# Performance work log

Hardware: AMD Instinct MI355X
Metric: run time of the kernel (lower is better)

## Reference

```python
import jax, jax.numpy as jnp
import numpy as np
import math
from itertools import combinations

SEQ_LEN = 8
SET_SIZE = 3
IN_DIM = 2048
OUT_DIM = 1152
WAY = 5
SHOT = 5
N_QUERIES = 200
PE_SCALE = 0.1
LN_EPS = 1e-5
NEG_INF = -1e30

TUPLES = np.array(list(combinations(range(SEQ_LEN), SET_SIZE)), dtype=np.int32)  # [56, 3]
TUPLES_LEN = TUPLES.shape[0]


def _positional_encoding(d_model, max_len):
    position = np.arange(max_len)[:, None].astype(np.float32)
    div_term = np.exp(np.arange(0, d_model, 2).astype(np.float32) * -(math.log(10000.0) / d_model))
    pe = np.zeros((max_len, d_model), dtype=np.float32)
    pe[:, 0::2] = np.sin(position * div_term) * PE_SCALE
    pe[:, 1::2] = np.cos(position * div_term) * PE_SCALE
    return jnp.asarray(pe)

PE = _positional_encoding(IN_DIM, int(SEQ_LEN * 1.5))


def setup_inputs() -> dict:
    key = jax.random.key(0)
    ks = jax.random.split(key, 6)
    support_set = jax.random.normal(ks[0], (WAY * SHOT, SEQ_LEN, IN_DIM), dtype=jnp.float32)
    queries = jax.random.normal(ks[1], (N_QUERIES, SEQ_LEN, IN_DIM), dtype=jnp.float32)
    support_labels = jnp.repeat(jnp.arange(WAY, dtype=jnp.int32), SHOT)  # [25]
    Wk = jax.random.normal(ks[2], (IN_DIM * SET_SIZE, OUT_DIM), dtype=jnp.float32) * 0.02
    bk = jnp.zeros((OUT_DIM,), dtype=jnp.float32)
    Wv = jax.random.normal(ks[3], (IN_DIM * SET_SIZE, OUT_DIM), dtype=jnp.float32) * 0.02
    bv = jnp.zeros((OUT_DIM,), dtype=jnp.float32)
    ln_g = jnp.ones((OUT_DIM,), dtype=jnp.float32)
    ln_b = jnp.zeros((OUT_DIM,), dtype=jnp.float32)
    return {"support_set": support_set, "support_labels": support_labels, "queries": queries,
            "Wk": Wk, "bk": bk, "Wv": Wv, "bv": bv, "ln_g": ln_g, "ln_b": ln_b}


def _layernorm(x, g, b):
    mu = jnp.mean(x, axis=-1, keepdims=True)
    var = jnp.var(x, axis=-1, keepdims=True)
    return (x - mu) * jax.lax.rsqrt(var + LN_EPS) * g + b


def _tuple_features(x):
    # x: [N, SEQ_LEN, IN_DIM]; add PE (dropout is identity at inference), gather frame tuples.
    n = x.shape[0]
    x = x + PE[None, :x.shape[1], :]
    return x[:, TUPLES, :].reshape(n, TUPLES_LEN, SET_SIZE * IN_DIM)  # [N, 56, 6144]


def reference(support_set, support_labels, queries, Wk, bk, Wv, bv, ln_g, ln_b):
    n_q = queries.shape[0]
    s_feat = _tuple_features(support_set)   # [S, T, 6144]
    q_feat = _tuple_features(queries)       # [Q, T, 6144]

    sk = _layernorm(s_feat @ Wk + bk, ln_g, ln_b)  # [S, T, D]
    qk = _layernorm(q_feat @ Wk + bk, ln_g, ln_b)  # [Q, T, D]
    sv = s_feat @ Wv + bv                           # [S, T, D]
    qv = q_feat @ Wv + bv                           # [Q, T, D]

    # scores between every query tuple and every support tuple
    scores = jnp.einsum('qtd,skd->qtsk', qk, sk) / math.sqrt(OUT_DIM)  # [Q, T, S, T]

    # per-class masked softmax over (support clips of class c) x (support tuples)
    class_mask = support_labels[None, :] == jnp.arange(WAY, dtype=support_labels.dtype)[:, None]  # [WAY, S]
    masked = scores[None] + jnp.where(class_mask[:, None, None, :, None], 0.0, NEG_INF)  # [WAY, Q, T, S, T]
    attn = jax.nn.softmax(masked.reshape(WAY, n_q, TUPLES_LEN, -1), axis=-1)
    attn = attn.reshape(WAY, n_q, TUPLES_LEN, -1, TUPLES_LEN)  # [WAY, Q, T, S, T]

    proto = jnp.einsum('cqtsk,skd->cqtd', attn, sv)  # [WAY, Q, T, D]
    diff = qv[None] - proto                           # [WAY, Q, T, D]
    dist = -jnp.sum(diff * diff, axis=(2, 3)) / TUPLES_LEN  # [WAY, Q]
    return dist.T  # logits [Q, WAY]
```

## Files before the change

kernel.cpp:

```cpp
#include <hip/hip_runtime.h>
#include <math.h>

#define SEQ_LEN 8
#define IN_DIM 2048
#define OUT_DIM 1152
#define NTUP 56
#define NSUP 25
#define NQ 200
#define WAY 5
#define SFRAMES 200
#define NFRAMES 1800
#define SROWS 1400
#define QROWS 11200
#define AT_STRIDE 1440
#define KC 288
#define ALD 296

typedef __attribute__((ext_vector_type(8))) short short8;
typedef __attribute__((ext_vector_type(4))) float f32x4;

__device__ __constant__ int TUP[NTUP][3] = {
{0,1,2},{0,1,3},{0,1,4},{0,1,5},{0,1,6},{0,1,7},
{0,2,3},{0,2,4},{0,2,5},{0,2,6},{0,2,7},
{0,3,4},{0,3,5},{0,3,6},{0,3,7},
{0,4,5},{0,4,6},{0,4,7},
{0,5,6},{0,5,7},
{0,6,7},
{1,2,3},{1,2,4},{1,2,5},{1,2,6},{1,2,7},
{1,3,4},{1,3,5},{1,3,6},{1,3,7},
{1,4,5},{1,4,6},{1,4,7},
{1,5,6},{1,5,7},
{1,6,7},
{2,3,4},{2,3,5},{2,3,6},{2,3,7},
{2,4,5},{2,4,6},{2,4,7},
{2,5,6},{2,5,7},
{2,6,7},
{3,4,5},{3,4,6},{3,4,7},
{3,5,6},{3,5,7},
{3,6,7},
{4,5,6},{4,5,7},
{4,6,7},
{5,6,7}};

__device__ __forceinline__ unsigned short f2bf(float x) {
  union { float f; unsigned int u; } v; v.f = x;
  unsigned int r = v.u + 0x7fffu + ((v.u >> 16) & 1u);
  return (unsigned short)(r >> 16);
}
__device__ __forceinline__ float bf2f(unsigned short s) {
  union { float f; unsigned int u; } v; v.u = ((unsigned int)s) << 16;
  return v.f;
}

__device__ __forceinline__ void gll16(const void* g, void* l) {
  __builtin_amdgcn_global_load_lds(
      (const __attribute__((address_space(1))) unsigned int*)g,
      (__attribute__((address_space(3))) unsigned int*)l, 16, 0, 0);
}

#define VMCNT(N) asm volatile("s_waitcnt vmcnt(" #N ")" ::: "memory")

__device__ __forceinline__ void pbar() {
  asm volatile("" ::: "memory");
  __builtin_amdgcn_s_barrier();
  asm volatile("" ::: "memory");
}

#define APB_OFF   0UL
#define WT_OFF    7372800UL
#define PB_OFF    35684352UL
#define QKB_OFF   60567552UL
#define SKB_OFF   86372352UL
#define QVB_OFF   89597952UL
#define SVB_OFF   115402752UL
#define G2_OFF    118628352UL
#define SCB_OFF   119457792UL
#define G1B_OFF   151713792UL
#define QNORM_OFF 183969792UL
#define RANK_OFF  184014592UL

__global__ __launch_bounds__(256) void k_pre(const float* __restrict__ S,
                                             const float* __restrict__ Q,
                                             const float* __restrict__ Wk,
                                             const float* __restrict__ Wv,
                                             const int* __restrict__ labels,
                                             unsigned short* __restrict__ APb,
                                             unsigned short* __restrict__ WT,
                                             int* __restrict__ rank,
                                             float* __restrict__ outz) {
  __shared__ float t[32][33];
  int b = blockIdx.x, tid = threadIdx.x;
  if (b < NFRAMES) {
    int frame = b;
    int e8 = tid * 8;
    int pos = frame & 7;
    const float c0 = -logf(10000.0f) / (float)IN_DIM;
    float pe[8];
#pragma unroll
    for (int p = 0; p < 4; ++p) {
      float dt = expf((float)(e8 + 2 * p) * c0);
      float arg = (float)pos * dt;
      pe[2 * p] = sinf(arg) * 0.1f;
      pe[2 * p + 1] = cosf(arg) * 0.1f;
    }
    const float* src = (frame < SFRAMES) ? (S + (size_t)frame * IN_DIM + e8)
                                         : (Q + (size_t)(frame - SFRAMES) * IN_DIM + e8);
    float4 x0 = ((const float4*)src)[0], x1 = ((const float4*)src)[1];
    short8 o;
    o[0] = (short)f2bf(x0.x + pe[0]); o[1] = (short)f2bf(x0.y + pe[1]);
    o[2] = (short)f2bf(x0.z + pe[2]); o[3] = (short)f2bf(x0.w + pe[3]);
    o[4] = (short)f2bf(x1.x + pe[4]); o[5] = (short)f2bf(x1.y + pe[5]);
    o[6] = (short)f2bf(x1.z + pe[6]); o[7] = (short)f2bf(x1.w + pe[7]);
    *(short8*)(APb + (size_t)frame * IN_DIM + e8) = o;
  } else if (b < NFRAMES + 13824) {
    int z = b - NFRAMES;
    int bz = z / (64 * 36); int rem = z % (64 * 36);
    int by = rem / 64, bx = rem % 64;
    int w = bz / 3, j = bz % 3;
    const float* W = w ? Wv : Wk;
    int k0 = bx * 32, d0 = by * 32;
    int tx = tid & 31, ty = tid >> 5;
#pragma unroll
    for (int i = 0; i < 4; ++i) {
      int k = k0 + ty + i * 8;
      t[ty + i * 8][tx] = W[(size_t)(j * IN_DIM + k) * OUT_DIM + d0 + tx];
    }
    __syncthreads();
    int colbase = w * 3456 + j * 1152 + d0;
#pragma unroll
    for (int i = 0; i < 4; ++i) {
      int d = ty + i * 8;
      WT[(size_t)(colbase + d) * IN_DIM + k0 + tx] = f2bf(t[tx][d]);
    }
  } else {
    for (int i = tid; i < NQ * WAY; i += 256) outz[i] = 0.f;
    if (tid == 0) {
      for (int s = 0; s < NSUP; ++s) {
        int r = 0;
        for (int s2 = 0; s2 < NSUP; ++s2)
          r += (labels[s2] < labels[s]) || (labels[s2] == labels[s] && s2 < s);
        rank[s] = r;
      }
    }
  }
}

__device__ __forceinline__ void mfma_core256(const short* __restrict__ A, int lda, int maxA,
                                             const short* __restrict__ B, int ldb, int maxB,
                                             int K, short* lds, f32x4 (&acc)[8][4]) {
  int tid = threadIdx.x;
  int lane = tid & 63, wave = tid >> 6;
  int wm = wave >> 1, wn = wave & 1;
  int col = lane & 15, quad = lane >> 4;
  int kq8 = (quad ^ ((col >> 1) & 3)) * 8;

  int rt_ = tid >> 2;
  int qo = ((tid & 3) ^ ((tid >> 3) & 3)) * 8;
  const short* a0p = A + (size_t)min(rt_,       maxA) * lda + qo;
  const short* a1p = A + (size_t)min(rt_ + 64,  maxA) * lda + qo;
  const short* a2p = A + (size_t)min(rt_ + 128, maxA) * lda + qo;
  const short* a3p = A + (size_t)min(rt_ + 192, maxA) * lda + qo;
  const short* b0p = B + (size_t)min(rt_,       maxB) * ldb + qo;
  const short* b1p = B + (size_t)min(rt_ + 64,  maxB) * ldb + qo;
  const int nt = K >> 5;

#define STAGE(t, cb)                                 \
  do {                                               \
    short* buf_ = lds + (cb);                        \
    int k0_ = (t) << 5;                              \
    gll16(a0p + k0_, buf_ + (size_t)tid * 8);        \
    gll16(a1p + k0_, buf_ + (size_t)(tid + 256) * 8);\
    gll16(a2p + k0_, buf_ + (size_t)(tid + 512) * 8);\
    gll16(a3p + k0_, buf_ + (size_t)(tid + 768) * 8);\
    gll16(b0p + k0_, buf_ + 8192 + (size_t)tid * 8); \
    gll16(b1p + k0_, buf_ + 8192 + (size_t)(tid + 256) * 8);\
  } while (0)

  STAGE(0, 0);
  STAGE(1, 12288);
  VMCNT(6);
  pbar();
  int c0 = 0, c1 = 12288, c2 = 24576;
  for (int t = 0; t < nt; ++t) {
    if (t + 2 < nt) STAGE(t + 2, c2);
    const short* As = lds + c0;
    const short* Bs = As + 8192;
    short8 af[8], bf[4];
#pragma unroll
    for (int i = 0; i < 8; ++i)
      af[i] = *(const short8*)(As + (wm * 128 + i * 16 + col) * 32 + kq8);
#pragma unroll
    for (int j = 0; j < 4; ++j)
      bf[j] = *(const short8*)(Bs + (wn * 64 + j * 16 + col) * 32 + kq8);
    __builtin_amdgcn_s_setprio(1);
#pragma unroll
    for (int i = 0; i < 8; ++i)
#pragma unroll
      for (int j = 0; j < 4; ++j)
        acc[i][j] = __builtin_amdgcn_mfma_f32_16x16x32_bf16(af[i], bf[j], acc[i][j], 0, 0, 0);
    __builtin_amdgcn_s_setprio(0);
    if (t + 2 < nt)      VMCNT(6);
    else if (t + 1 < nt) VMCNT(0);
    pbar();
    int tmp = c0; c0 = c1; c1 = c2; c2 = tmp;
  }
#undef STAGE
}

__global__ __launch_bounds__(256, 2) void k_gemm1(const unsigned short* __restrict__ APb,
                                                  const unsigned short* __restrict__ WT,
                                                  unsigned short* __restrict__ Pb) {
  __shared__ short lds[36864];
  int o = blockIdx.x;
  int L = (o & 7) * 54 + (o >> 3);
  int rt = L / 54, ct = L % 54;
  int row0 = rt << 8, col0 = ct << 7;
  f32x4 acc[8][4];
#pragma unroll
  for (int i = 0; i < 8; ++i)
#pragma unroll
    for (int j = 0; j < 4; ++j) acc[i][j] = (f32x4)(0.f);
  mfma_core256((const short*)APb + (size_t)row0 * IN_DIM, IN_DIM, min(255, NFRAMES - 1 - row0),
               (const short*)WT + (size_t)col0 * IN_DIM, IN_DIM, 127,
               IN_DIM, lds, acc);
  int lane = threadIdx.x & 63, wave = threadIdx.x >> 6;
  int wm = wave >> 1, wn = wave & 1, col = lane & 15, quad = lane >> 4;
#pragma unroll
  for (int i = 0; i < 8; ++i)
#pragma unroll
    for (int r = 0; r < 4; ++r) {
      int gr = row0 + wm * 128 + i * 16 + quad * 4 + r;
      if (gr >= NFRAMES) continue;
#pragma unroll
      for (int j = 0; j < 4; ++j)
        Pb[(size_t)gr * 6912 + col0 + wn * 64 + j * 16 + col] = f2bf(acc[i][j][r]);
    }
}

__global__ __launch_bounds__(256) void k_combine(const unsigned short* __restrict__ Pb,
                                                 const float* __restrict__ bk,
                                                 const float* __restrict__ bv,
                                                 const float* __restrict__ g,
                                                 const float* __restrict__ bb,
                                                 const int* __restrict__ rank,
                                                 unsigned short* __restrict__ SKb,
                                                 unsigned short* __restrict__ QKb,
                                                 unsigned short* __restrict__ SVb,
                                                 unsigned short* __restrict__ QVb,
                                                 float* __restrict__ qnorm) {
  __shared__ short L[8 * 3456];
  int n = blockIdx.x, w = blockIdx.y;
  int tid = threadIdx.x;
  bool sup = n < NSUP;
  int fbase = sup ? n * SEQ_LEN : SFRAMES + (n - NSUP) * SEQ_LEN;
  for (int i = 0; i < 14; ++i) {
    int idx = tid + 256 * i;
    if (idx < 3456) {
      int fr = idx / 432, off = (idx - fr * 432) * 8;
      *(short8*)(L + fr * 3456 + off) =
          *(const short8*)(Pb + (size_t)(fbase + fr) * 6912 + w * 3456 + off);
    }
  }
  __syncthreads();
  int wave = tid >> 6, lane = tid & 63;
  const float* bias = w ? bv : bk;
  float2 bi[9], gg[9], bbv[9];
#pragma unroll
  for (int i = 0; i < 9; ++i) {
    int p = lane + 64 * i;
    bi[i] = *(const float2*)(bias + 2 * p);
    if (w == 0) {
      gg[i] = *(const float2*)(g + 2 * p);
      bbv[i] = *(const float2*)(bb + 2 * p);
    }
  }
  int obase = sup ? rank[n] * NTUP : (n - NSUP) * NTUP;
  const unsigned int* Lu = (const unsigned int*)L;
  for (int t = wave; t < NTUP; t += 4) {
    int b0 = (TUP[t][0] * 3456) >> 1;
    int b1 = (TUP[t][1] * 3456 + 1152) >> 1;
    int b2 = (TUP[t][2] * 3456 + 2304) >> 1;
    float va[18];
    float sum = 0.f, sq = 0.f;
#pragma unroll
    for (int i = 0; i < 9; ++i) {
      int p = lane + 64 * i;
      unsigned int u0 = Lu[b0 + p], u1 = Lu[b1 + p], u2 = Lu[b2 + p];
      float a = bf2f((unsigned short)u0) + bf2f((unsigned short)u1) +
                bf2f((unsigned short)u2) + bi[i].x;
      float b = bf2f((unsigned short)(u0 >> 16)) + bf2f((unsigned short)(u1 >> 16)) +
                bf2f((unsigned short)(u2 >> 16)) + bi[i].y;
      va[2 * i] = a; va[2 * i + 1] = b;
      sum += a + b;
      sq += a * a + b * b;
    }
#pragma unroll
    for (int o = 32; o; o >>= 1) {
      sum += __shfl_xor(sum, o);
      sq += __shfl_xor(sq, o);
    }
    int orow = obase + t;
    if (w == 0) {
      float mean = sum * (1.f / OUT_DIM);
      float var = sq * (1.f / OUT_DIM) - mean * mean;
      float inv = rsqrtf(var + 1e-5f);
      unsigned short* outp = (sup ? SKb : QKb) + (size_t)orow * OUT_DIM;
#pragma unroll
      for (int i = 0; i < 9; ++i) {
        int p = lane + 64 * i;
        unsigned int lo = f2bf((va[2 * i] - mean) * inv * gg[i].x + bbv[i].x);
        unsigned int hi = f2bf((va[2 * i + 1] - mean) * inv * gg[i].y + bbv[i].y);
        *(unsigned int*)(outp + 2 * p) = lo | (hi << 16);
      }
    } else {
      unsigned short* outp = (sup ? SVb : QVb) + (size_t)orow * OUT_DIM;
#pragma unroll
      for (int i = 0; i < 9; ++i) {
        int p = lane + 64 * i;
        unsigned int lo = f2bf(va[2 * i]);
        unsigned int hi = f2bf(va[2 * i + 1]);
        *(unsigned int*)(outp + 2 * p) = lo | (hi << 16);
      }
      if (!sup && lane == 0) qnorm[orow] = sq;
    }
  }
}

__global__ __launch_bounds__(256, 2) void k_rowgemm(const unsigned short* __restrict__ QKb,
                                                    const unsigned short* __restrict__ SKb,
                                                    const unsigned short* __restrict__ QVb,
                                                    const unsigned short* __restrict__ SVb,
                                                    unsigned short* __restrict__ SCb,
                                                    unsigned short* __restrict__ G1b,
                                                    unsigned short* __restrict__ G2) {
  __shared__ short lds[36864];
  int o = blockIdx.x;
  int xcd = o & 7, idx = o >> 3;
  int L = (xcd < 6 ? xcd * 125 : 750 + (xcd - 6) * 124) + idx;
  f32x4 acc[8][4];
#pragma unroll
  for (int i = 0; i < 8; ++i)
#pragma unroll
    for (int j = 0; j < 4; ++j) acc[i][j] = (f32x4)(0.f);
  int lane = threadIdx.x & 63, wave = threadIdx.x >> 6;
  int wm = wave >> 1, wn = wave & 1, col = lane & 15, quad = lane >> 4;

  if (L < 968) {
    int g1 = L >= 484; int l = g1 ? L - 484 : L;
    int rt = l / 11, ct = l % 11;
    int row0 = rt << 8, col0 = ct << 7;
    const unsigned short* Am = g1 ? QVb : QKb;
    const unsigned short* Bm = g1 ? SVb : SKb;
    mfma_core256((const short*)Am + (size_t)row0 * OUT_DIM, OUT_DIM, min(255, QROWS - 1 - row0),
                 (const short*)Bm + (size_t)col0 * OUT_DIM, OUT_DIM, min(127, SROWS - 1 - col0),
                 OUT_DIM, lds, acc);
    unsigned short* outp = g1 ? G1b : SCb;
    const float scl = g1 ? 1.0f : 0.029462782549439483f;
#pragma unroll
    for (int i = 0; i < 8; ++i)
#pragma unroll
      for (int r = 0; r < 4; ++r) {
        int gr = row0 + wm * 128 + i * 16 + quad * 4 + r;
        if (gr >= QROWS) continue;
#pragma unroll
        for (int j = 0; j < 4; ++j) {
          int gc = col0 + wn * 64 + j * 16 + col;
          if (gc < SROWS) {
            int c = gc / 280;
            outp[(size_t)gr * AT_STRIDE + gc + c * 8] = f2bf(acc[i][j][r] * scl);
          }
        }
      }
  } else {
    int l = L - 968;
    int c = l / 6, rem = l % 6;
    int rt = rem / 3, ct = rem % 3;
    int i0 = rt << 8, j0 = ct << 7;
    const short* base = (const short*)SVb + (size_t)c * 280 * OUT_DIM;
    mfma_core256(base + (size_t)i0 * OUT_DIM, OUT_DIM, 279 - i0,
                 base + (size_t)j0 * OUT_DIM, OUT_DIM, min(127, 279 - j0),
                 OUT_DIM, lds, acc);
    unsigned short* g2c = G2 + (size_t)c * KC * KC;
#pragma unroll
    for (int i = 0; i < 8; ++i)
#pragma unroll
      for (int r = 0; r < 4; ++r) {
        int gi = i0 + wm * 128 + i * 16 + quad * 4 + r;
        if (gi >= KC) continue;
#pragma unroll
        for (int j = 0; j < 4; ++j) {
          int gj = j0 + wn * 64 + j * 16 + col;
          if (gj < KC) g2c[(size_t)gi * KC + gj] = f2bf(acc[i][j][r]);
        }
      }
  }
}

__global__ __launch_bounds__(256) void k_attn(const unsigned short* __restrict__ SCb,
                                              const unsigned short* __restrict__ G1b,
                                              const unsigned short* __restrict__ G2,
                                              const float* __restrict__ qnorm,
                                              float* __restrict__ out) {
  __shared__ short attn[64 * ALD];
  __shared__ float T2n[64];
  __shared__ float Sarr[64];
  __shared__ float rowsum[64];
  __shared__ float val[64];
  int r0 = blockIdx.x * 64, c = blockIdx.y;
  int tid = threadIdx.x;

  int lr = tid >> 2, h = tid & 3;
  const unsigned short* ps = SCb + (size_t)(r0 + lr) * AT_STRIDE + c * KC;
  const unsigned short* pg = G1b + (size_t)(r0 + lr) * AT_STRIDE + c * KC;
  short8 sv[9];
  float mx = -INFINITY;
#pragma unroll
  for (int i = 0; i < 9; ++i) {
    int v = h * 9 + i;
    if (v < 35) {
      sv[i] = *(const short8*)(ps + v * 8);
#pragma unroll
      for (int j = 0; j < 8; ++j) mx = fmaxf(mx, bf2f((unsigned short)sv[i][j]));
    }
  }
  mx = fmaxf(mx, __shfl_xor(mx, 1));
  mx = fmaxf(mx, __shfl_xor(mx, 2));
  float sum = 0.f, t2 = 0.f;
#pragma unroll
  for (int i = 0; i < 9; ++i) {
    int v = h * 9 + i;
    if (v < 35) {
      short8 gv8 = *(const short8*)(pg + v * 8);
      short8 e8;
#pragma unroll
      for (int j = 0; j < 8; ++j) {
        float e = __expf(bf2f((unsigned short)sv[i][j]) - mx);
        sum += e;
        t2 += e * bf2f((unsigned short)gv8[j]);
        e8[j] = (short)f2bf(e);
      }
      *(short8*)(attn + lr * ALD + v * 8) = e8;
    } else {
      *(short8*)(attn + lr * ALD + v * 8) = (short8)0;
    }
  }
  sum += __shfl_xor(sum, 1); sum += __shfl_xor(sum, 2);
  t2 += __shfl_xor(t2, 1); t2 += __shfl_xor(t2, 2);
  if (h == 0) { Sarr[lr] = sum; T2n[lr] = t2; }
  if (tid < 64) rowsum[tid] = 0.f;
  __syncthreads();

  int lane = tid & 63, wave = tid >> 6;
  int col = lane & 15, quad = lane >> 4;
  const short* G2c = (const short*)G2 + (size_t)c * KC * KC;
  float part[4][4] = {};
  for (int j0 = 0; j0 < KC; j0 += 64) {
    int ncols = min(64, KC - j0);
    if (wave * 16 < ncols) {
      const short* brow = G2c + (size_t)(j0 + wave * 16 + col) * KC + quad * 8;
      f32x4 acc[4];
#pragma unroll
      for (int i = 0; i < 4; ++i) acc[i] = (f32x4)(0.f);
      for (int kq = 0; kq < 9; ++kq) {
        short8 bf = *(const short8*)(brow + kq * 32);
#pragma unroll
        for (int i = 0; i < 4; ++i) {
          short8 af = *(const short8*)(attn + (i * 16 + col) * ALD + kq * 32 + quad * 8);
          acc[i] = __builtin_amdgcn_mfma_f32_16x16x32_bf16(af, bf, acc[i], 0, 0, 0);
        }
      }
      int gcol = j0 + wave * 16 + col;
#pragma unroll
      for (int i = 0; i < 4; ++i)
#pragma unroll
        for (int r = 0; r < 4; ++r)
          part[i][r] += bf2f((unsigned short)attn[(i * 16 + quad * 4 + r) * ALD + gcol]) *
                        acc[i][r];
    }
  }
#pragma unroll
  for (int i = 0; i < 4; ++i)
#pragma unroll
    for (int r = 0; r < 4; ++r) {
      float s = part[i][r];
      s += __shfl_xor(s, 1); s += __shfl_xor(s, 2);
      s += __shfl_xor(s, 4); s += __shfl_xor(s, 8);
      if (col == 0) atomicAdd(&rowsum[i * 16 + quad * 4 + r], s);
    }
  __syncthreads();

  if (tid < 64) {
    float S = Sarr[tid], invS = 1.f / S;
    val[tid] = qnorm[r0 + tid] - 2.f * T2n[tid] * invS + rowsum[tid] * invS * invS;
  }
  __syncthreads();
  if (tid < 3) {
    int q = r0 / NTUP + tid;
    int lo = max(q * NTUP, r0), hi = min(q * NTUP + NTUP, r0 + 64);
    if (lo < hi && q < NQ) {
      float s = 0.f;
      for (int r = lo; r < hi; ++r) s += val[r - r0];
      atomicAdd(&out[q * WAY + c], -s * (1.f / NTUP));
    }
  }
}

extern "C" void kernel_launch(void* const* d_in, const int* in_sizes, int n_in,
                              void* d_out, int out_size, void* d_ws, size_t ws_size,
                              hipStream_t stream) {
  const float* support = (const float*)d_in[0];
  const int* labels = (const int*)d_in[1];
  const float* queries = (const float*)d_in[2];
  const float* Wk = (const float*)d_in[3];
  const float* bk = (const float*)d_in[4];
  const float* Wv = (const float*)d_in[5];
  const float* bv = (const float*)d_in[6];
  const float* ln_g = (const float*)d_in[7];
  const float* ln_b = (const float*)d_in[8];
  float* out = (float*)d_out;
  char* w8 = (char*)d_ws;

  unsigned short* APb = (unsigned short*)(w8 + APB_OFF);
  unsigned short* WT = (unsigned short*)(w8 + WT_OFF);
  unsigned short* Pb = (unsigned short*)(w8 + PB_OFF);
  unsigned short* QKb = (unsigned short*)(w8 + QKB_OFF);
  unsigned short* SKb = (unsigned short*)(w8 + SKB_OFF);
  unsigned short* QVb = (unsigned short*)(w8 + QVB_OFF);
  unsigned short* SVb = (unsigned short*)(w8 + SVB_OFF);
  unsigned short* G2 = (unsigned short*)(w8 + G2_OFF);
  unsigned short* SCb = (unsigned short*)(w8 + SCB_OFF);
  unsigned short* G1b = (unsigned short*)(w8 + G1B_OFF);
  float* QNORM = (float*)(w8 + QNORM_OFF);
  int* RANK = (int*)(w8 + RANK_OFF);

  k_pre<<<dim3(NFRAMES + 13824 + 1), dim3(256), 0, stream>>>(support, queries, Wk, Wv,
                                                             labels, APb, WT, RANK, out);
  k_gemm1<<<dim3(432), dim3(256), 0, stream>>>(APb, WT, Pb);
  k_combine<<<dim3(225, 2), dim3(256), 0, stream>>>(Pb, bk, bv, ln_g, ln_b, RANK,
                                                    SKb, QKb, SVb, QVb, QNORM);
  k_rowgemm<<<dim3(998), dim3(256), 0, stream>>>(QKb, SKb, QVb, SVb, SCb, G1b, G2);
  k_attn<<<dim3(175, 5), dim3(256), 0, stream>>>(SCb, G1b, G2, QNORM, out);
}
```

Measured before the change: 342.0 us.

## Compute query-support value Gram from per-frame projection products instead of tuple rows

Instead of forming the full 11200x1400 QV·SV^T GEMM over tuple rows, the query and support value projections are packed per frame (three 1152-wide chunks per frame) and a much smaller 4800x600 frame-level GEMM is computed. A new assembly kernel then reconstructs each tuple-pair dot product by summing the frame-chunk products plus the bias cross-terms. This exploits the tuple structure to drop about 484 GEMM tiles, and the tuple-level QV matrix is no longer written. In exchange it adds two extra kernel launches, an fp32 intermediate buffer, and a scattered assembly pass.

```diff
diff --git a/kernel.cpp b/kernel.cpp
--- a/kernel.cpp
+++ b/kernel.cpp
@@ -71,7 +71,10 @@
 #define PB_OFF    35684352UL
 #define QKB_OFF   60567552UL
 #define SKB_OFF   86372352UL
-#define QVB_OFF   89597952UL
+#define AQ_OFF    89597952UL
+#define AS_OFF    100657152UL
+#define PVB_OFF   102039552UL
+#define H_OFF     102061312UL
 #define SVB_OFF   115402752UL
 #define G2_OFF    118628352UL
 #define SCB_OFF   119457792UL
@@ -237,6 +240,34 @@
     }
 }
 
+__global__ __launch_bounds__(256) void k_pack(const unsigned short* __restrict__ Pb,
+                                              const float* __restrict__ bv,
+                                              const int* __restrict__ rank,
+                                              unsigned short* __restrict__ Aq,
+                                              unsigned short* __restrict__ As,
+                                              float* __restrict__ pvb) {
+  int fr = blockIdx.x, tid = threadIdx.x;
+  const unsigned short* src = Pb + (size_t)fr * 6912 + 3456;
+  unsigned short* dst;
+  if (fr < SFRAMES) {
+    int n = fr >> 3, f = fr & 7;
+    dst = As + ((size_t)rank[n] * 8 + f) * 3456;
+  } else {
+    dst = Aq + (size_t)(fr - SFRAMES) * 3456;
+  }
+  for (int i = tid; i < 432; i += 256)
+    *(short8*)(dst + i * 8) = *(const short8*)(src + i * 8);
+  int wave = tid >> 6, lane = tid & 63;
+  if (wave < 3) {
+    float s = 0.f;
+    for (int k = lane; k < OUT_DIM; k += 64)
+      s += bf2f(src[wave * 1152 + k]) * bv[k];
+#pragma unroll
+    for (int o = 32; o; o >>= 1) s += __shfl_xor(s, o);
+    if (lane == 0) pvb[fr * 3 + wave] = s;
+  }
+}
+
 __global__ __launch_bounds__(256) void k_combine(const unsigned short* __restrict__ Pb,
                                                  const float* __restrict__ bk,
                                                  const float* __restrict__ bv,
@@ -246,7 +277,6 @@
                                                  unsigned short* __restrict__ SKb,
                                                  unsigned short* __restrict__ QKb,
                                                  unsigned short* __restrict__ SVb,
-                                                 unsigned short* __restrict__ QVb,
                                                  float* __restrict__ qnorm) {
   __shared__ short L[8 * 3456];
   int n = blockIdx.x, w = blockIdx.y;
@@ -312,8 +342,8 @@
         unsigned int hi = f2bf((va[2 * i + 1] - mean) * inv * gg[i].y + bbv[i].y);
         *(unsigned int*)(outp + 2 * p) = lo | (hi << 16);
       }
-    } else {
-      unsigned short* outp = (sup ? SVb : QVb) + (size_t)orow * OUT_DIM;
+    } else if (sup) {
+      unsigned short* outp = SVb + (size_t)orow * OUT_DIM;
 #pragma unroll
       for (int i = 0; i < 9; ++i) {
         int p = lane + 64 * i;
@@ -321,22 +351,24 @@
         unsigned int hi = f2bf(va[2 * i + 1]);
         *(unsigned int*)(outp + 2 * p) = lo | (hi << 16);
       }
-      if (!sup && lane == 0) qnorm[orow] = sq;
+    } else {
+      if (lane == 0) qnorm[orow] = sq;
     }
   }
 }
 
 __global__ __launch_bounds__(256, 2) void k_rowgemm(const unsigned short* __restrict__ QKb,
                                                     const unsigned short* __restrict__ SKb,
-                                                    const unsigned short* __restrict__ QVb,
                                                     const unsigned short* __restrict__ SVb,
+                                                    const unsigned short* __restrict__ Aq,
+                                                    const unsigned short* __restrict__ As,
                                                     unsigned short* __restrict__ SCb,
-                                                    unsigned short* __restrict__ G1b,
+                                                    float* __restrict__ H,
                                                     unsigned short* __restrict__ G2) {
   __shared__ short lds[36864];
   int o = blockIdx.x;
   int xcd = o & 7, idx = o >> 3;
-  int L = (xcd < 6 ? xcd * 125 : 750 + (xcd - 6) * 124) + idx;
+  int L = (xcd == 0 ? idx : 77 + (xcd - 1) * 76 + idx);
   f32x4 acc[8][4];
 #pragma unroll
   for (int i = 0; i < 8; ++i)
@@ -345,17 +377,13 @@
   int lane = threadIdx.x & 63, wave = threadIdx.x >> 6;
   int wm = wave >> 1, wn = wave & 1, col = lane & 15, quad = lane >> 4;
 
-  if (L < 968) {
-    int g1 = L >= 484; int l = g1 ? L - 484 : L;
-    int rt = l / 11, ct = l % 11;
+  if (L < 484) {
+    int rt = L / 11, ct = L % 11;
     int row0 = rt << 8, col0 = ct << 7;
-    const unsigned short* Am = g1 ? QVb : QKb;
-    const unsigned short* Bm = g1 ? SVb : SKb;
-    mfma_core256((const short*)Am + (size_t)row0 * OUT_DIM, OUT_DIM, min(255, QROWS - 1 - row0),
-                 (const short*)Bm + (size_t)col0 * OUT_DIM, OUT_DIM, min(127, SROWS - 1 - col0),
+    mfma_core256((const short*)QKb + (size_t)row0 * OUT_DIM, OUT_DIM, min(255, QROWS - 1 - row0),
+                 (const short*)SKb + (size_t)col0 * OUT_DIM, OUT_DIM, min(127, SROWS - 1 - col0),
                  OUT_DIM, lds, acc);
-    unsigned short* outp = g1 ? G1b : SCb;
-    const float scl = g1 ? 1.0f : 0.029462782549439483f;
+    const float scl = 0.029462782549439483f;
 #pragma unroll
     for (int i = 0; i < 8; ++i)
 #pragma unroll
@@ -367,12 +395,31 @@
           int gc = col0 + wn * 64 + j * 16 + col;
           if (gc < SROWS) {
             int c = gc / 280;
-            outp[(size_t)gr * AT_STRIDE + gc + c * 8] = f2bf(acc[i][j][r] * scl);
+            SCb[(size_t)gr * AT_STRIDE + gc + c * 8] = f2bf(acc[i][j][r] * scl);
           }
         }
       }
+  } else if (L < 579) {
+    int l = L - 484;
+    int rt = l / 5, ct = l % 5;
+    int row0 = rt << 8, col0 = ct << 7;
+    mfma_core256((const short*)Aq + (size_t)row0 * OUT_DIM, OUT_DIM, min(255, 4799 - row0),
+                 (const short*)As + (size_t)col0 * OUT_DIM, OUT_DIM, min(127, 599 - col0),
+                 OUT_DIM, lds, acc);
+#pragma unroll
+    for (int i = 0; i < 8; ++i)
+#pragma unroll
+      for (int r = 0; r < 4; ++r) {
+        int gr = row0 + wm * 128 + i * 16 + quad * 4 + r;
+        if (gr >= 4800) continue;
+#pragma unroll
+        for (int j = 0; j < 4; ++j) {
+          int gc = col0 + wn * 64 + j * 16 + col;
+          if (gc < 600) H[(size_t)gr * 640 + gc] = acc[i][j][r];
+        }
+      }
   } else {
-    int l = L - 968;
+    int l = L - 579;
     int c = l / 6, rem = l % 6;
     int rt = rem / 3, ct = rem % 3;
     int i0 = rt << 8, j0 = ct << 7;
@@ -393,6 +440,57 @@
           if (gj < KC) g2c[(size_t)gi * KC + gj] = f2bf(acc[i][j][r]);
         }
       }
+  }
+}
+
+__global__ __launch_bounds__(256) void k_g1asm(const float* __restrict__ H,
+                                               const float* __restrict__ pvb,
+                                               const float* __restrict__ bv,
+                                               const int* __restrict__ rank,
+                                               unsigned short* __restrict__ G1b) {
+  __shared__ float Hs[24][24];
+  __shared__ float M1[56][24];
+  __shared__ float ubv[56], wbv[56];
+  __shared__ float bb2s;
+  __shared__ int inv[25];
+  int qc = blockIdx.x, r = blockIdx.y;
+  int tid = threadIdx.x;
+  if (tid < 25) inv[rank[tid]] = tid;
+  if (tid < 64) {
+    float s = 0.f;
+    for (int k = tid; k < OUT_DIM; k += 64) { float b = bv[k]; s += b * b; }
+#pragma unroll
+    for (int o = 32; o; o >>= 1) s += __shfl_xor(s, o);
+    if (tid == 0) bb2s = s;
+  }
+  for (int i = tid; i < 576; i += 256) {
+    int a = i / 24, b = i % 24;
+    Hs[a][b] = H[(size_t)(qc * 24 + a) * 640 + r * 24 + b];
+  }
+  __syncthreads();
+  int n = inv[r];
+  if (tid < 56) {
+    float s = 0.f, w = 0.f;
+#pragma unroll
+    for (int j = 0; j < 3; ++j) {
+      s += pvb[(SFRAMES + qc * 8 + TUP[tid][j]) * 3 + j];
+      w += pvb[(n * 8 + TUP[tid][j]) * 3 + j];
+    }
+    ubv[tid] = s; wbv[tid] = w;
+  }
+  for (int i = tid; i < 1344; i += 256) {
+    int t = i / 24, b = i % 24;
+    M1[t][b] = Hs[TUP[t][0] * 3 + 0][b] + Hs[TUP[t][1] * 3 + 1][b] + Hs[TUP[t][2] * 3 + 2][b];
+  }
+  __syncthreads();
+  float bb2 = bb2s;
+  int c = r / 5;
+  size_t colbase = (size_t)c * KC + (r % 5) * 56;
+  for (int i = tid; i < 3136; i += 256) {
+    int t = i / 56, tp = i % 56;
+    float v = M1[t][TUP[tp][0] * 3 + 0] + M1[t][TUP[tp][1] * 3 + 1] +
+              M1[t][TUP[tp][2] * 3 + 2] + ubv[t] + wbv[tp] + bb2;
+    G1b[(size_t)(qc * 56 + t) * AT_STRIDE + colbase + tp] = f2bf(v);
   }
 }
 
@@ -525,7 +623,10 @@
   unsigned short* Pb = (unsigned short*)(w8 + PB_OFF);
   unsigned short* QKb = (unsigned short*)(w8 + QKB_OFF);
   unsigned short* SKb = (unsigned short*)(w8 + SKB_OFF);
-  unsigned short* QVb = (unsigned short*)(w8 + QVB_OFF);
+  unsigned short* Aq = (unsigned short*)(w8 + AQ_OFF);
+  unsigned short* As = (unsigned short*)(w8 + AS_OFF);
+  float* PVB = (float*)(w8 + PVB_OFF);
+  float* H = (float*)(w8 + H_OFF);
   unsigned short* SVb = (unsigned short*)(w8 + SVB_OFF);
   unsigned short* G2 = (unsigned short*)(w8 + G2_OFF);
   unsigned short* SCb = (unsigned short*)(w8 + SCB_OFF);
@@ -536,8 +637,10 @@
   k_pre<<<dim3(NFRAMES + 13824 + 1), dim3(256), 0, stream>>>(support, queries, Wk, Wv,
                                                              labels, APb, WT, RANK, out);
   k_gemm1<<<dim3(432), dim3(256), 0, stream>>>(APb, WT, Pb);
+  k_pack<<<dim3(NFRAMES), dim3(256), 0, stream>>>(Pb, bv, RANK, Aq, As, PVB);
   k_combine<<<dim3(225, 2), dim3(256), 0, stream>>>(Pb, bk, bv, ln_g, ln_b, RANK,
-                                                    SKb, QKb, SVb, QVb, QNORM);
-  k_rowgemm<<<dim3(998), dim3(256), 0, stream>>>(QKb, SKb, QVb, SVb, SCb, G1b, G2);
+                                                    SKb, QKb, SVb, QNORM);
+  k_rowgemm<<<dim3(609), dim3(256), 0, stream>>>(QKb, SKb, SVb, Aq, As, SCb, H, G2);
+  k_g1asm<<<dim3(200, 25), dim3(256), 0, stream>>>(H, PVB, bv, RANK, G1b);
   k_attn<<<dim3(175, 5), dim3(256), 0, stream>>>(SCb, G1b, G2, QNORM, out);
 }
```

Result: slower. 370.6 us (+8.4%).
